# Performance work log

Hardware: AMD Instinct MI355X
Metric: run time of the kernel (lower is better)

The kernel has to match this reference:

```python
import jax, jax.numpy as jnp
import numpy as np
import math

B, S, D, O_DIM = 8, 2048, 1024, 1024

def setup_inputs() -> dict:
    key = jax.random.key(0)
    ks = jax.random.split(key, 4)
    scale = 1.0 / math.sqrt(D)
    return {
        "x": jax.random.normal(ks[0], (B, S, D), dtype=jnp.float32),
        "Wq": jax.random.normal(ks[1], (D, O_DIM), dtype=jnp.float32) * scale,
        "bq": jnp.zeros((O_DIM,), dtype=jnp.float32),
        "Wk": jax.random.normal(ks[2], (D, O_DIM), dtype=jnp.float32) * scale,
        "bk": jnp.zeros((O_DIM,), dtype=jnp.float32),
        "Wv": jax.random.normal(ks[3], (D, O_DIM), dtype=jnp.float32) * scale,
        "bv": jnp.zeros((O_DIM,), dtype=jnp.float32),
    }

def reference(x, Wq, bq, Wk, bk, Wv, bv):
    o_dim = Wq.shape[1]
    q = x @ Wq + bq  # [B,S,O]
    k = x @ Wk + bk
    v = x @ Wv + bv
    scores = jnp.einsum('bid,bjd->bij', q, k) / jnp.sqrt(jnp.float32(o_dim))
    n = scores.shape[1]
    # causal additive mask: upper triangle (j > i) gets -1e20 added
    causal = jnp.tril(jnp.ones((n, n), dtype=scores.dtype))
    scores = scores + (1.0 - causal) * (-1e20)
    probs = jax.nn.softmax(scores, axis=-1)
    return jnp.einsum('bij,bjd->bid', probs, v)
```

## Files before the change

kernel.cpp:

```cpp
#include <hip/hip_runtime.h>

#define BM 128
#define BN 128
#define BK 32

typedef unsigned short u16;
typedef unsigned int u32;
typedef __attribute__((ext_vector_type(8))) short short8;
typedef __attribute__((ext_vector_type(4))) float floatx4;

__device__ __forceinline__ u16 f2bf(float f) {
  u32 u = __float_as_uint(f);
  return (u16)((u + 0x7FFFu + ((u >> 16) & 1u)) >> 16);
}

__device__ __forceinline__ float bf2f(u16 b) {
  return __uint_as_float(((u32)b) << 16);
}

__device__ __forceinline__ void gload16(const void* g, void* l) {
  __builtin_amdgcn_global_load_lds((const __attribute__((address_space(1))) void*)g,
                                   (__attribute__((address_space(3))) void*)l, 16, 0, 0);
}

template<int BIAS_MODE, bool OUT_BF16, bool CAUSAL, bool KLIMIT, bool SWZ>
__global__ __launch_bounds__(256)
void gemm_nt(const u16* __restrict__ A, int lda, long strideA,
             const u16* __restrict__ B, int ldb, long strideB,
             void* __restrict__ Cv, int ldc, long strideC,
             const float* __restrict__ bias, float scale,
             int M, int N, int K)
{
  int bx = blockIdx.x;
  if (SWZ) {
    const int c = gridDim.x >> 3;
    bx = (bx & 7) * c + (bx >> 3);
  }
  const int rb = blockIdx.y * BM;
  const int cb = bx * BN;
  if (CAUSAL && cb > rb + (BM - 1)) return;

  A += (long)blockIdx.z * strideA;
  B += (long)blockIdx.z * strideB;
  const long coff = (long)blockIdx.z * strideC;

  __shared__ u16 As[BM * BK];
  __shared__ u16 Bs[BN * BK];

  const int t = threadIdx.x;
  const int lane = t & 63;
  const int wid = t >> 6;
  const int wr = wid >> 1, wc = wid & 1;

  floatx4 acc[4][4];
#pragma unroll
  for (int i = 0; i < 4; ++i)
#pragma unroll
    for (int j = 0; j < 4; ++j) acc[i][j] = (floatx4)(0.0f);

  const int srow = t >> 2;
  const int schunk = (t & 3) ^ ((srow >> 1) & 3);
  const u16* Ag0 = A + (long)(rb + srow) * lda + schunk * 8;
  const u16* Ag1 = A + (long)(rb + srow + 64) * lda + schunk * 8;
  const u16* Bg0 = B + (long)(cb + srow) * ldb + schunk * 8;
  const u16* Bg1 = B + (long)(cb + srow + 64) * ldb + schunk * 8;
  char* AsW = (char*)As + wid * 1024;
  char* BsW = (char*)Bs + wid * 1024;

  const int arow = wr * 64 + (lane & 15);
  const int brow = wc * 64 + (lane & 15);
  const int rchunk = lane >> 4;
  int aoff[4], boff[4];
#pragma unroll
  for (int i = 0; i < 4; ++i) {
    const int ra = arow + i * 16;
    aoff[i] = ra * 64 + ((rchunk ^ ((ra >> 1) & 3)) * 16);
    const int rbq = brow + i * 16;
    boff[i] = rbq * 64 + ((rchunk ^ ((rbq >> 1) & 3)) * 16);
  }

  int kend = K;
  if (KLIMIT) kend = (rb + BM < K) ? (rb + BM) : K;
  const int ktiles = kend / BK;

  for (int kt = 0; kt < ktiles; ++kt) {
    const long ko = (long)kt * BK;
    gload16(Ag0 + ko, AsW);
    gload16(Ag1 + ko, AsW + 4096);
    gload16(Bg0 + ko, BsW);
    gload16(Bg1 + ko, BsW + 4096);
    __syncthreads();
    short8 af[4], bfr[4];
#pragma unroll
    for (int i = 0; i < 4; ++i) {
      af[i]  = *(const short8*)((const char*)As + aoff[i]);
      bfr[i] = *(const short8*)((const char*)Bs + boff[i]);
    }
#pragma unroll
    for (int mi = 0; mi < 4; ++mi)
#pragma unroll
      for (int nj = 0; nj < 4; ++nj)
        acc[mi][nj] = __builtin_amdgcn_mfma_f32_16x16x32_bf16(af[mi], bfr[nj], acc[mi][nj], 0, 0, 0);
    __syncthreads();
  }

#pragma unroll
  for (int mi = 0; mi < 4; ++mi) {
    const int r0 = rb + wr * 64 + mi * 16 + (lane >> 4) * 4;
#pragma unroll
    for (int nj = 0; nj < 4; ++nj) {
      const int c = cb + wc * 64 + nj * 16 + (lane & 15);
      float bc = 0.0f;
      if (BIAS_MODE == 1) bc = bias[c];
#pragma unroll
      for (int e = 0; e < 4; ++e) {
        const int r = r0 + e;
        float val = acc[mi][nj][e] * scale + bc;
        if (BIAS_MODE == 2) val += bias[r];
        const long idx = coff + (long)r * ldc + c;
        if (OUT_BF16) ((u16*)Cv)[idx] = f2bf(val);
        else          ((float*)Cv)[idx] = val;
      }
    }
  }
}

__global__ __launch_bounds__(256)
void softmax_causal_bf16(u16* __restrict__ Pp, int n, long stride)
{
  const int i = blockIdx.x;
  u16* row = Pp + (long)blockIdx.y * stride + (long)i * n;
  const int t = threadIdx.x;
  const int lane = t & 63, wid = t >> 6;
  const int jb = t * 8;

  float v[8];
  const bool any = (jb <= i);
  if (any) {
    short8 sv = *(const short8*)(row + jb);
#pragma unroll
    for (int e = 0; e < 8; ++e) v[e] = bf2f((u16)sv[e]);
  } else {
#pragma unroll
    for (int e = 0; e < 8; ++e) v[e] = 0.0f;
  }

  float mx = -3.0e38f;
#pragma unroll
  for (int e = 0; e < 8; ++e) if (any && jb + e <= i) mx = fmaxf(mx, v[e]);
#pragma unroll
  for (int off = 32; off > 0; off >>= 1) mx = fmaxf(mx, __shfl_xor(mx, off));
  __shared__ float red[8];
  if (lane == 0) red[wid] = mx;
  __syncthreads();
  mx = fmaxf(fmaxf(red[0], red[1]), fmaxf(red[2], red[3]));

  float s = 0.0f;
#pragma unroll
  for (int e = 0; e < 8; ++e) {
    float p = (any && jb + e <= i) ? __expf(v[e] - mx) : 0.0f;
    v[e] = p; s += p;
  }
#pragma unroll
  for (int off = 32; off > 0; off >>= 1) s += __shfl_xor(s, off);
  if (lane == 0) red[4 + wid] = s;
  __syncthreads();
  s = red[4] + red[5] + red[6] + red[7];
  const float inv = 1.0f / s;

  short8 o;
#pragma unroll
  for (int e = 0; e < 8; ++e) o[e] = (short)f2bf(v[e] * inv);
  *(short8*)(row + jb) = o;
}

__global__ __launch_bounds__(256)
void transpose_conv(const float* __restrict__ W, u16* __restrict__ WT, int dim)
{
  __shared__ float tile[32][33];
  const int tx = threadIdx.x & 31;
  const int ty = threadIdx.x >> 5;
  const int c0 = blockIdx.x * 32;
  const int r0 = blockIdx.y * 32;
#pragma unroll
  for (int i = 0; i < 4; ++i)
    tile[ty + 8 * i][tx] = W[(long)(r0 + ty + 8 * i) * dim + c0 + tx];
  __syncthreads();
#pragma unroll
  for (int i = 0; i < 4; ++i)
    WT[(long)(c0 + ty + 8 * i) * dim + r0 + tx] = f2bf(tile[tx][ty + 8 * i]);
}

__global__ __launch_bounds__(256)
void conv_bf16(const float* __restrict__ X, u16* __restrict__ Xb, long n8)
{
  const long i = (long)blockIdx.x * 256 + threadIdx.x;
  if (i >= n8) return;
  const float4* s = (const float4*)X + i * 2;
  float4 a = s[0], b = s[1];
  short8 o;
  o[0] = (short)f2bf(a.x); o[1] = (short)f2bf(a.y);
  o[2] = (short)f2bf(a.z); o[3] = (short)f2bf(a.w);
  o[4] = (short)f2bf(b.x); o[5] = (short)f2bf(b.y);
  o[6] = (short)f2bf(b.z); o[7] = (short)f2bf(b.w);
  ((short8*)Xb)[i] = o;
}

__global__ __launch_bounds__(256)
void pack_bias2(const float* __restrict__ b0, const float* __restrict__ b1,
                float* __restrict__ dst, int n)
{
  const int i = blockIdx.x * 256 + threadIdx.x;
  if (i < n) dst[i] = b0[i];
  else if (i < 2 * n) dst[i] = b1[i - n];
}

extern "C" void kernel_launch(void* const* d_in, const int* in_sizes, int n_in,
                              void* d_out, int out_size, void* d_ws, size_t ws_size,
                              hipStream_t stream)
{
  const int Bb = 8, S = 2048, Dd = 1024, Od = 1024;
  const int M = Bb * S;

  const float* x  = (const float*)d_in[0];
  const float* Wq = (const float*)d_in[1];
  const float* bq = (const float*)d_in[2];
  const float* Wk = (const float*)d_in[3];
  const float* bk = (const float*)d_in[4];
  const float* Wv = (const float*)d_in[5];
  const float* bv = (const float*)d_in[6];
  float* out = (float*)d_out;

  char* ws = (char*)d_ws;
  u16* xb   = (u16*)(ws);
  u16* qk   = (u16*)(ws + 33554432L);
  u16* vT   = (u16*)(ws + 100663296L);
  u16* WqkT = (u16*)(ws + 134217728L);
  u16* WvT  = (u16*)(ws + 138412032L);
  float* bqk = (float*)(ws + 140509184L);
  const size_t attn_base = 140517376UL;
  u16* scores = (u16*)(ws + attn_base);

  conv_bf16<<<dim3(8192), dim3(256), 0, stream>>>(x, xb, (long)M * Dd / 8);
  transpose_conv<<<dim3(32, 32), dim3(256), 0, stream>>>(Wq, WqkT, Dd);
  transpose_conv<<<dim3(32, 32), dim3(256), 0, stream>>>(Wk, WqkT + (long)Od * Dd, Dd);
  transpose_conv<<<dim3(32, 32), dim3(256), 0, stream>>>(Wv, WvT, Dd);
  pack_bias2<<<dim3(8), dim3(256), 0, stream>>>(bq, bk, bqk, Od);

  dim3 blk(256);
  gemm_nt<1, true, false, false, true><<<dim3(2 * Od / BN, M / BM, 1), blk, 0, stream>>>(
      xb, Dd, 0L, WqkT, Dd, 0L, qk, 2 * Od, 0L, bqk, 1.0f, M, 2 * Od, Dd);
  gemm_nt<2, true, false, false, true><<<dim3(M / BN, Od / BM, 1), blk, 0, stream>>>(
      WvT, Dd, 0L, xb, Dd, 0L, vT, M, 0L, bv, 1.0f, Od, M, Dd);

  const u16* qb = qk;
  const u16* kb = qk + Od;
  const int ldqk = 2 * Od;
  const long strideQK = (long)S * ldqk;
  const long sS = (long)S * S;

  int g = 1;
  for (int cand = 8; cand >= 1; cand >>= 1) {
    if (ws_size >= attn_base + (size_t)cand * sS * sizeof(u16)) { g = cand; break; }
  }

  const float sc = 0.03125f;
  for (int b0 = 0; b0 < Bb; b0 += g) {
    const int gz = (b0 + g <= Bb) ? g : (Bb - b0);
    gemm_nt<0, true, true, false, false><<<dim3(S / BN, S / BM, gz), blk, 0, stream>>>(
        qb + (long)b0 * strideQK, ldqk, strideQK,
        kb + (long)b0 * strideQK, ldqk, strideQK,
        scores, S, sS, nullptr, sc, S, S, Od);
    softmax_causal_bf16<<<dim3(S, gz), blk, 0, stream>>>(scores, S, sS);
    gemm_nt<0, false, false, true, false><<<dim3(Od / BN, S / BM, gz), blk, 0, stream>>>(
        scores, S, sS, vT + (long)b0 * S, M, (long)S,
        out + (long)b0 * S * Od, Od, (long)S * Od, nullptr, 1.0f, S, Od, S);
  }
}
```

Before: 479.7 us.

## Add XCD-aware block swizzles, reverse PV row order, reuse xb for scores

```diff
diff --git a/kernel.cpp b/kernel.cpp
--- a/kernel.cpp
+++ b/kernel.cpp
@@ -23,7 +23,7 @@
                                    (__attribute__((address_space(3))) void*)l, 16, 0, 0);
 }
 
-template<int BIAS_MODE, bool OUT_BF16, bool CAUSAL, bool KLIMIT, bool SWZ>
+template<int BIAS_MODE, bool OUT_BF16, bool CAUSAL, bool KLIMIT, int SWZ>
 __global__ __launch_bounds__(256)
 void gemm_nt(const u16* __restrict__ A, int lda, long strideA,
              const u16* __restrict__ B, int ldb, long strideB,
@@ -32,11 +32,22 @@
              int M, int N, int K)
 {
   int bx = blockIdx.x;
-  if (SWZ) {
+  int by = blockIdx.y;
+  if (SWZ == 1) {
     const int c = gridDim.x >> 3;
     bx = (bx & 7) * c + (bx >> 3);
-  }
-  const int rb = blockIdx.y * BM;
+  } else if (SWZ == 2) {
+    const u32 gx = gridDim.x;
+    const u32 flat = (u32)by * gx + (u32)bx;
+    const u32 j = flat & 7u;
+    const u32 w = flat >> 3;
+    const u32 rpx = gridDim.y >> 3;
+    by = (int)(j * rpx + w / gx);
+    bx = (int)(w % gx);
+  } else if (SWZ == 3) {
+    by = gridDim.y - 1 - by;
+  }
+  const int rb = by * BM;
   const int cb = bx * BN;
   if (CAUSAL && cb > rb + (BM - 1)) return;
 
@@ -239,7 +250,6 @@
   u16* WvT  = (u16*)(ws + 138412032L);
   float* bqk = (float*)(ws + 140509184L);
   const size_t attn_base = 140517376UL;
-  u16* scores = (u16*)(ws + attn_base);
 
   conv_bf16<<<dim3(8192), dim3(256), 0, stream>>>(x, xb, (long)M * Dd / 8);
   transpose_conv<<<dim3(32, 32), dim3(256), 0, stream>>>(Wq, WqkT, Dd);
@@ -248,9 +258,9 @@
   pack_bias2<<<dim3(8), dim3(256), 0, stream>>>(bq, bk, bqk, Od);
 
   dim3 blk(256);
-  gemm_nt<1, true, false, false, true><<<dim3(2 * Od / BN, M / BM, 1), blk, 0, stream>>>(
+  gemm_nt<1, true, false, false, 2><<<dim3(2 * Od / BN, M / BM, 1), blk, 0, stream>>>(
       xb, Dd, 0L, WqkT, Dd, 0L, qk, 2 * Od, 0L, bqk, 1.0f, M, 2 * Od, Dd);
-  gemm_nt<2, true, false, false, true><<<dim3(M / BN, Od / BM, 1), blk, 0, stream>>>(
+  gemm_nt<2, true, false, false, 1><<<dim3(M / BN, Od / BM, 1), blk, 0, stream>>>(
       WvT, Dd, 0L, xb, Dd, 0L, vT, M, 0L, bv, 1.0f, Od, M, Dd);
 
   const u16* qb = qk;
@@ -259,20 +269,25 @@
   const long strideQK = (long)S * ldqk;
   const long sS = (long)S * S;
 
-  int g = 1;
-  for (int cand = 8; cand >= 1; cand >>= 1) {
-    if (ws_size >= attn_base + (size_t)cand * sS * sizeof(u16)) { g = cand; break; }
+  u16* scores;
+  int g;
+  if (ws_size >= attn_base + 8UL * (size_t)sS * sizeof(u16)) {
+    scores = (u16*)(ws + attn_base);
+    g = 8;
+  } else {
+    scores = xb;
+    g = 4;
   }
 
   const float sc = 0.03125f;
   for (int b0 = 0; b0 < Bb; b0 += g) {
     const int gz = (b0 + g <= Bb) ? g : (Bb - b0);
-    gemm_nt<0, true, true, false, false><<<dim3(S / BN, S / BM, gz), blk, 0, stream>>>(
+    gemm_nt<0, true, true, false, 0><<<dim3(S / BN, S / BM, gz), blk, 0, stream>>>(
         qb + (long)b0 * strideQK, ldqk, strideQK,
         kb + (long)b0 * strideQK, ldqk, strideQK,
         scores, S, sS, nullptr, sc, S, S, Od);
     softmax_causal_bf16<<<dim3(S, gz), blk, 0, stream>>>(scores, S, sS);
-    gemm_nt<0, false, false, true, false><<<dim3(Od / BN, S / BM, gz), blk, 0, stream>>>(
+    gemm_nt<0, false, false, true, 3><<<dim3(Od / BN, S / BM, gz), blk, 0, stream>>>(
         scores, S, sS, vT + (long)b0 * S, M, (long)S,
         out + (long)b0 * S * Od, Od, (long)S * Od, nullptr, 1.0f, S, Od, S);
   }
```

New measurement: 474.3 us. About the same (-1.1%).
